# Performance work log

Measured on AMD Instinct MI355X. Metric: run time of the kernel, lower is better.

## Reference

```python
import jax, jax.numpy as jnp
import numpy as np

B, T, H, W, D = 64, 512, 768, 256, 256  # batch, tokens, bert hidden, max words, embedding_dim


def setup_inputs() -> dict:
    key = jax.random.key(0)
    k1, k2, k3 = jax.random.split(key, 3)
    hidden_states = jax.random.normal(k1, (B, T, H), dtype=jnp.float32)
    # word_ids from a fast tokenizer are nondecreasing within a sentence
    word_ids = jnp.sort(jax.random.randint(k2, (B, T), 0, W), axis=-1)
    proj_w = jax.random.normal(k3, (H, D), dtype=jnp.float32) / np.sqrt(H).astype(np.float32)
    proj_b = jnp.zeros((D,), dtype=jnp.float32)
    return {"hidden_states": hidden_states, "word_ids": word_ids,
            "proj_w": proj_w, "proj_b": proj_b}


def _segment_mean(h, wid):
    # h: [T, H], wid: [T]. Invalid ids (<0 or >=W, i.e. special/pad tokens)
    # are routed to a dump segment W that is sliced away.
    idx = jnp.where((wid >= 0) & (wid < W), wid, W)
    sums = jax.ops.segment_sum(h, idx, num_segments=W + 1)[:W]          # [W, H]
    counts = jax.ops.segment_sum(jnp.ones((h.shape[0],), h.dtype), idx,
                                 num_segments=W + 1)[:W]                 # [W]
    # torch.clamp(counts, min=1) -> padded/empty words stay zero
    return sums / jnp.maximum(counts, 1.0)[:, None]


def reference(hidden_states, word_ids, proj_w, proj_b):
    # token-to-word scatter-mean pooling, vectorized over batch
    word_emb = jax.vmap(_segment_mean)(hidden_states, word_ids)  # [B, W, H]
    # final linear projection to embedding_dim
    return jnp.einsum('bwh,hd->bwd', word_emb, proj_w) + proj_b  # [B, W, D]
```

## Files before the change

### kernel.cpp

```cpp
#include <hip/hip_runtime.h>


#define NB 64
#define NT 512
#define NH 768
#define NW 256
#define ND 256
#define PAD 8
#define ROWE (NH + PAD)

typedef __attribute__((ext_vector_type(8))) short short8;
typedef __attribute__((ext_vector_type(4))) float f32x4;
typedef __attribute__((ext_vector_type(4))) float float4v;
typedef __attribute__((ext_vector_type(4))) unsigned short ushort4v;

__device__ __forceinline__ unsigned short f2bf(float f) {
    union { float f; unsigned u; } v; v.f = f;
    unsigned r = v.u + 0x7fffu + ((v.u >> 16) & 1u);
    return (unsigned short)(r >> 16);
}

__global__ void prep_wt2(const float* __restrict__ w, unsigned short* __restrict__ wt2) {
    __shared__ float tile[32][33];
    const int tid = threadIdx.x, n = blockIdx.x;
    const int tx = tid & 31, ty = tid >> 5;
    const int k0 = (n % 24) * 32, n0 = (n / 24) * 32;
    #pragma unroll
    for (int i = 0; i < 4; ++i)
        tile[ty + 8 * i][tx] = w[(size_t)(k0 + ty + 8 * i) * ND + n0 + tx];
    __syncthreads();
    if (tid < 128) {
        const int cc = tid & 31, q = tid >> 5;
        const int col = n0 + cc;
        ushort4v u0, u1;
        #pragma unroll
        for (int j = 0; j < 4; ++j) u0[j] = f2bf(tile[q * 8 + j][cc]);
        #pragma unroll
        for (int j = 0; j < 4; ++j) u1[j] = f2bf(tile[q * 8 + 4 + j][cc]);
        size_t off = (((size_t)(col >> 4) * 96 + (k0 >> 3) + q) * 16 + (col & 15)) * 8;
        *(ushort4v*)&wt2[off]     = u0;
        *(ushort4v*)&wt2[off + 4] = u1;
    }
}

__global__ __launch_bounds__(256, 3)
void fused(const float* __restrict__ hs, const int* __restrict__ wid,
           const unsigned short* __restrict__ wt2, const float* __restrict__ pb,
           float* __restrict__ out) {
    __shared__ unsigned short A[32][ROWE];
    __shared__ int swid[NT];
    __shared__ int sb[33];

    const int tid = threadIdx.x, bid = blockIdx.x;
    const int wave = tid >> 6, lane = tid & 63;
    const int b = bid >> 3, w0 = (bid & 7) * 32;

    swid[tid]       = wid[b * NT + tid];
    swid[tid + 256] = wid[b * NT + tid + 256];
    __syncthreads();
    if (tid <= 32) {
        int v = w0 + tid, lo = 0, hi = NT;
        while (lo < hi) { int mid = (lo + hi) >> 1; if (swid[mid] < v) lo = mid + 1; else hi = mid; }
        sb[tid] = lo;
    }
    __syncthreads();

    const float* base = hs + (size_t)b * NT * NH + lane * 4;
    #pragma unroll 1
    for (int pp = 0; pp < 4; ++pp) {
        const int p = wave * 4 + pp;
        const int s = sb[2 * p], m = sb[2 * p + 1], e = sb[2 * p + 2];

        float4v a0c0 = {0,0,0,0}, a0c1 = {0,0,0,0}, a0c2 = {0,0,0,0};
        float4v a1c0 = {0,0,0,0}, a1c1 = {0,0,0,0}, a1c2 = {0,0,0,0};
#define ROUTE(t, v0, v1, v2) {                                                \
        if ((t) < m) {                                                        \
            _Pragma("unroll") for (int q = 0; q < 4; ++q) {                   \
                a0c0[q] += (v0)[q]; a0c1[q] += (v1)[q]; a0c2[q] += (v2)[q]; } \
        } else {                                                              \
            _Pragma("unroll") for (int q = 0; q < 4; ++q) {                   \
                a1c0[q] += (v0)[q]; a1c1[q] += (v1)[q]; a1c2[q] += (v2)[q]; } \
        }                                                                     \
    }
        int t = s;
        for (; t + 2 <= e; t += 2) {
            float4v v[2][3];
            #pragma unroll
            for (int u = 0; u < 2; ++u) {
                const float* p2 = base + (size_t)(t + u) * NH;
                v[u][0] = *(const float4v*)(p2);
                v[u][1] = *(const float4v*)(p2 + 256);
                v[u][2] = *(const float4v*)(p2 + 512);
            }
            #pragma unroll
            for (int u = 0; u < 2; ++u) ROUTE(t + u, v[u][0], v[u][1], v[u][2]);
        }
        if (t < e) {
            const float* p2 = base + (size_t)t * NH;
            float4v v0 = *(const float4v*)(p2);
            float4v v1 = *(const float4v*)(p2 + 256);
            float4v v2 = *(const float4v*)(p2 + 512);
            ROUTE(t, v0, v1, v2);
        }
#undef ROUTE
        int c0n = m - s; if (c0n < 1) c0n = 1;
        int c1n = e - m; if (c1n < 1) c1n = 1;
        const float s0 = 1.0f / (float)c0n, s1 = 1.0f / (float)c1n;
        ushort4v u;
        #pragma unroll
        for (int q = 0; q < 4; ++q) u[q] = f2bf(a0c0[q] * s0);
        *(ushort4v*)&A[2 * p][lane * 4] = u;
        #pragma unroll
        for (int q = 0; q < 4; ++q) u[q] = f2bf(a0c1[q] * s0);
        *(ushort4v*)&A[2 * p][256 + lane * 4] = u;
        #pragma unroll
        for (int q = 0; q < 4; ++q) u[q] = f2bf(a0c2[q] * s0);
        *(ushort4v*)&A[2 * p][512 + lane * 4] = u;
        #pragma unroll
        for (int q = 0; q < 4; ++q) u[q] = f2bf(a1c0[q] * s1);
        *(ushort4v*)&A[2 * p + 1][lane * 4] = u;
        #pragma unroll
        for (int q = 0; q < 4; ++q) u[q] = f2bf(a1c1[q] * s1);
        *(ushort4v*)&A[2 * p + 1][256 + lane * 4] = u;
        #pragma unroll
        for (int q = 0; q < 4; ++q) u[q] = f2bf(a1c2[q] * s1);
        *(ushort4v*)&A[2 * p + 1][512 + lane * 4] = u;
    }
    __syncthreads();

    const int cl = lane & 15, kg = lane >> 4;
    const int c0w = wave * 64;
    const unsigned short* bgp = wt2 + (size_t)(wave * 4) * 12288 + kg * 128 + cl * 8;

    short8 a0[2], a1[2], b0[4], b1[4];
    f32x4 acc[2][4];
    #pragma unroll
    for (int mt = 0; mt < 2; ++mt)
        #pragma unroll
        for (int nt = 0; nt < 4; ++nt)
            #pragma unroll
            for (int r = 0; r < 4; ++r) acc[mt][nt][r] = 0.f;

#define LDA(d, ks) { d[0] = *(const short8*)&A[cl][(ks) * 32 + kg * 8];       \
                     d[1] = *(const short8*)&A[16 + cl][(ks) * 32 + kg * 8]; }
#define LDB(d, ks) { _Pragma("unroll")                                        \
                     for (int nt = 0; nt < 4; ++nt)                           \
                         d[nt] = *(const short8*)(bgp + nt * 12288 + (ks) * 512); }
#define MM(a, bb) { _Pragma("unroll")                                         \
                    for (int mt = 0; mt < 2; ++mt)                            \
                        _Pragma("unroll")                                     \
                        for (int nt = 0; nt < 4; ++nt)                        \
                            acc[mt][nt] = __builtin_amdgcn_mfma_f32_16x16x32_bf16(a[mt], bb[nt], acc[mt][nt], 0, 0, 0); }

    LDA(a0, 0); LDB(b0, 0);
    #pragma unroll 1
    for (int i = 0; i < 12; ++i) {
        const int ks = 2 * i;
        LDA(a1, ks + 1); LDB(b1, ks + 1);
        MM(a0, b0);
        if (i < 11) { LDA(a0, ks + 2); LDB(b0, ks + 2); }
        MM(a1, b1);
    }
#undef LDA
#undef LDB
#undef MM

    float bv[4];
    #pragma unroll
    for (int nt = 0; nt < 4; ++nt) bv[nt] = pb[c0w + nt * 16 + cl];

    #pragma unroll
    for (int mt = 0; mt < 2; ++mt)
        #pragma unroll
        for (int nt = 0; nt < 4; ++nt)
            #pragma unroll
            for (int r = 0; r < 4; ++r)
                out[((size_t)b * NW + w0 + mt * 16 + kg * 4 + r) * ND + c0w + nt * 16 + cl]
                    = acc[mt][nt][r] + bv[nt];
}

extern "C" void kernel_launch(void* const* d_in, const int* in_sizes, int n_in,
                              void* d_out, int out_size, void* d_ws, size_t ws_size,
                              hipStream_t stream) {
    const float* hs  = (const float*)d_in[0];
    const int*   wid = (const int*)d_in[1];
    const float* pw  = (const float*)d_in[2];
    const float* pb  = (const float*)d_in[3];
    float* out = (float*)d_out;

    unsigned short* wt2 = (unsigned short*)d_ws;

    prep_wt2<<<192, 256, 0, stream>>>(pw, wt2);
    fused<<<NB * (NW / 32), 256, 0, stream>>>(hs, wid, wt2, pb, out);
}
```

Before: 36.05 us.

## Interleave segment pooling and MFMA projection in three K-chunk passes

Splits the hidden dimension into three 256-wide chunks. For each chunk the kernel pools tokens into the LDS A tile and then runs the MFMA GEMM on that slice, so pooling of later chunks can overlap with matrix math across waves and fewer float accumulators stay live. The token loop now unrolls by four over a single chunk instead of by two over three chunks. The cost is three extra barriers and re-reading the segment bounds per pass. There is no barrier between the MFMA reads of one pass and the next pass's writes, but they touch disjoint columns, so this is safe.

```diff
diff --git a/kernel.cpp b/kernel.cpp
--- a/kernel.cpp
+++ b/kernel.cpp
@@ -65,74 +65,10 @@
     }
     __syncthreads();
 
-    const float* base = hs + (size_t)b * NT * NH + lane * 4;
-    #pragma unroll 1
-    for (int pp = 0; pp < 4; ++pp) {
-        const int p = wave * 4 + pp;
-        const int s = sb[2 * p], m = sb[2 * p + 1], e = sb[2 * p + 2];
-
-        float4v a0c0 = {0,0,0,0}, a0c1 = {0,0,0,0}, a0c2 = {0,0,0,0};
-        float4v a1c0 = {0,0,0,0}, a1c1 = {0,0,0,0}, a1c2 = {0,0,0,0};
-#define ROUTE(t, v0, v1, v2) {                                                \
-        if ((t) < m) {                                                        \
-            _Pragma("unroll") for (int q = 0; q < 4; ++q) {                   \
-                a0c0[q] += (v0)[q]; a0c1[q] += (v1)[q]; a0c2[q] += (v2)[q]; } \
-        } else {                                                              \
-            _Pragma("unroll") for (int q = 0; q < 4; ++q) {                   \
-                a1c0[q] += (v0)[q]; a1c1[q] += (v1)[q]; a1c2[q] += (v2)[q]; } \
-        }                                                                     \
-    }
-        int t = s;
-        for (; t + 2 <= e; t += 2) {
-            float4v v[2][3];
-            #pragma unroll
-            for (int u = 0; u < 2; ++u) {
-                const float* p2 = base + (size_t)(t + u) * NH;
-                v[u][0] = *(const float4v*)(p2);
-                v[u][1] = *(const float4v*)(p2 + 256);
-                v[u][2] = *(const float4v*)(p2 + 512);
-            }
-            #pragma unroll
-            for (int u = 0; u < 2; ++u) ROUTE(t + u, v[u][0], v[u][1], v[u][2]);
-        }
-        if (t < e) {
-            const float* p2 = base + (size_t)t * NH;
-            float4v v0 = *(const float4v*)(p2);
-            float4v v1 = *(const float4v*)(p2 + 256);
-            float4v v2 = *(const float4v*)(p2 + 512);
-            ROUTE(t, v0, v1, v2);
-        }
-#undef ROUTE
-        int c0n = m - s; if (c0n < 1) c0n = 1;
-        int c1n = e - m; if (c1n < 1) c1n = 1;
-        const float s0 = 1.0f / (float)c0n, s1 = 1.0f / (float)c1n;
-        ushort4v u;
-        #pragma unroll
-        for (int q = 0; q < 4; ++q) u[q] = f2bf(a0c0[q] * s0);
-        *(ushort4v*)&A[2 * p][lane * 4] = u;
-        #pragma unroll
-        for (int q = 0; q < 4; ++q) u[q] = f2bf(a0c1[q] * s0);
-        *(ushort4v*)&A[2 * p][256 + lane * 4] = u;
-        #pragma unroll
-        for (int q = 0; q < 4; ++q) u[q] = f2bf(a0c2[q] * s0);
-        *(ushort4v*)&A[2 * p][512 + lane * 4] = u;
-        #pragma unroll
-        for (int q = 0; q < 4; ++q) u[q] = f2bf(a1c0[q] * s1);
-        *(ushort4v*)&A[2 * p + 1][lane * 4] = u;
-        #pragma unroll
-        for (int q = 0; q < 4; ++q) u[q] = f2bf(a1c1[q] * s1);
-        *(ushort4v*)&A[2 * p + 1][256 + lane * 4] = u;
-        #pragma unroll
-        for (int q = 0; q < 4; ++q) u[q] = f2bf(a1c2[q] * s1);
-        *(ushort4v*)&A[2 * p + 1][512 + lane * 4] = u;
-    }
-    __syncthreads();
-
     const int cl = lane & 15, kg = lane >> 4;
     const int c0w = wave * 64;
     const unsigned short* bgp = wt2 + (size_t)(wave * 4) * 12288 + kg * 128 + cl * 8;
-
-    short8 a0[2], a1[2], b0[4], b1[4];
+    short8 a0f, a1f, b0f[4], b1f[4];
     f32x4 acc[2][4];
     #pragma unroll
     for (int mt = 0; mt < 2; ++mt)
@@ -141,29 +77,84 @@
             #pragma unroll
             for (int r = 0; r < 4; ++r) acc[mt][nt][r] = 0.f;
 
-#define LDA(d, ks) { d[0] = *(const short8*)&A[cl][(ks) * 32 + kg * 8];       \
-                     d[1] = *(const short8*)&A[16 + cl][(ks) * 32 + kg * 8]; }
+#define LDA2(d0, d1, ks) { d0 = *(const short8*)&A[cl][(ks) * 32 + kg * 8];   \
+                           d1 = *(const short8*)&A[16 + cl][(ks) * 32 + kg * 8]; }
 #define LDB(d, ks) { _Pragma("unroll")                                        \
                      for (int nt = 0; nt < 4; ++nt)                           \
                          d[nt] = *(const short8*)(bgp + nt * 12288 + (ks) * 512); }
-#define MM(a, bb) { _Pragma("unroll")                                         \
-                    for (int mt = 0; mt < 2; ++mt)                            \
-                        _Pragma("unroll")                                     \
-                        for (int nt = 0; nt < 4; ++nt)                        \
-                            acc[mt][nt] = __builtin_amdgcn_mfma_f32_16x16x32_bf16(a[mt], bb[nt], acc[mt][nt], 0, 0, 0); }
+#define MM2(aa0, aa1, bb) { _Pragma("unroll")                                 \
+                    for (int nt = 0; nt < 4; ++nt) {                          \
+                        acc[0][nt] = __builtin_amdgcn_mfma_f32_16x16x32_bf16(aa0, bb[nt], acc[0][nt], 0, 0, 0); \
+                        acc[1][nt] = __builtin_amdgcn_mfma_f32_16x16x32_bf16(aa1, bb[nt], acc[1][nt], 0, 0, 0); } }
 
-    LDA(a0, 0); LDB(b0, 0);
+    const float* base0 = hs + (size_t)b * NT * NH + lane * 4;
+
+    short8 a0b, a1b;
     #pragma unroll 1
-    for (int i = 0; i < 12; ++i) {
-        const int ks = 2 * i;
-        LDA(a1, ks + 1); LDB(b1, ks + 1);
-        MM(a0, b0);
-        if (i < 11) { LDA(a0, ks + 2); LDB(b0, ks + 2); }
-        MM(a1, b1);
+    for (int pass = 0; pass < 3; ++pass) {
+        const float* base = base0 + pass * 256;
+        #pragma unroll 1
+        for (int pp = 0; pp < 4; ++pp) {
+            const int p = wave * 4 + pp;
+            const int s = sb[2 * p], m = sb[2 * p + 1], e = sb[2 * p + 2];
+            float4v A0 = {0,0,0,0}, A1 = {0,0,0,0};
+            int t = s;
+            for (; t + 4 <= e; t += 4) {
+                float4v v0 = *(const float4v*)(base + (size_t)(t    ) * NH);
+                float4v v1 = *(const float4v*)(base + (size_t)(t + 1) * NH);
+                float4v v2 = *(const float4v*)(base + (size_t)(t + 2) * NH);
+                float4v v3 = *(const float4v*)(base + (size_t)(t + 3) * NH);
+                #pragma unroll
+                for (int q = 0; q < 4; ++q) {
+                    if (t     < m) A0[q] += v0[q]; else A1[q] += v0[q];
+                }
+                #pragma unroll
+                for (int q = 0; q < 4; ++q) {
+                    if (t + 1 < m) A0[q] += v1[q]; else A1[q] += v1[q];
+                }
+                #pragma unroll
+                for (int q = 0; q < 4; ++q) {
+                    if (t + 2 < m) A0[q] += v2[q]; else A1[q] += v2[q];
+                }
+                #pragma unroll
+                for (int q = 0; q < 4; ++q) {
+                    if (t + 3 < m) A0[q] += v3[q]; else A1[q] += v3[q];
+                }
+            }
+            for (; t < e; ++t) {
+                float4v v = *(const float4v*)(base + (size_t)t * NH);
+                #pragma unroll
+                for (int q = 0; q < 4; ++q) {
+                    if (t < m) A0[q] += v[q]; else A1[q] += v[q];
+                }
+            }
+            int c0n = m - s; if (c0n < 1) c0n = 1;
+            int c1n = e - m; if (c1n < 1) c1n = 1;
+            const float s0 = 1.0f / (float)c0n, s1 = 1.0f / (float)c1n;
+            ushort4v u;
+            #pragma unroll
+            for (int q = 0; q < 4; ++q) u[q] = f2bf(A0[q] * s0);
+            *(ushort4v*)&A[2 * p][pass * 256 + lane * 4] = u;
+            #pragma unroll
+            for (int q = 0; q < 4; ++q) u[q] = f2bf(A1[q] * s1);
+            *(ushort4v*)&A[2 * p + 1][pass * 256 + lane * 4] = u;
+        }
+        __syncthreads();
+
+        const int ks0 = pass * 8;
+        LDA2(a0f, a0b, ks0); LDB(b0f, ks0);
+        #pragma unroll
+        for (int i = 0; i < 4; ++i) {
+            const int ks = ks0 + 2 * i;
+            LDA2(a1f, a1b, ks + 1); LDB(b1f, ks + 1);
+            MM2(a0f, a0b, b0f);
+            if (i < 3) { LDA2(a0f, a0b, ks + 2); LDB(b0f, ks + 2); }
+            MM2(a1f, a1b, b1f);
+        }
     }
-#undef LDA
+#undef LDA2
 #undef LDB
-#undef MM
+#undef MM2
 
     float bv[4];
     #pragma unroll
```

Result: slower. 41.83 us (+16.0%).
